# Optimization experiments

Hardware: AMD Instinct MI355X
Metric: run time of the kernel (lower is better)

## Reference

```python
import jax, jax.numpy as jnp
import numpy as np

HIDDEN = 1024
HEADS = 16
HEAD_DIM = HIDDEN // HEADS
SCALE = float(np.sqrt(HEAD_DIM))


def setup_inputs() -> dict:
    key = jax.random.key(0)
    ks = jax.random.split(key, 9)
    B, S = 4, 8192
    std = 1.0 / np.sqrt(HIDDEN)
    x = jax.random.normal(ks[0], (B, S, HIDDEN), dtype=jnp.float32)
    Wq = jax.random.normal(ks[1], (HIDDEN, HIDDEN), dtype=jnp.float32) * std
    Wk = jax.random.normal(ks[2], (HIDDEN, HIDDEN), dtype=jnp.float32) * std
    Wv = jax.random.normal(ks[3], (HIDDEN, HIDDEN), dtype=jnp.float32) * std
    Wo = jax.random.normal(ks[4], (HIDDEN, HIDDEN), dtype=jnp.float32) * std
    bq = jax.random.normal(ks[5], (HIDDEN,), dtype=jnp.float32) * std
    bk = jax.random.normal(ks[6], (HIDDEN,), dtype=jnp.float32) * std
    bv = jax.random.normal(ks[7], (HIDDEN,), dtype=jnp.float32) * std
    bo = jax.random.normal(ks[8], (HIDDEN,), dtype=jnp.float32) * std
    return {"x": x, "Wq": Wq, "bq": bq, "Wk": Wk, "bk": bk,
            "Wv": Wv, "bv": bv, "Wo": Wo, "bo": bo}


def reference(x, Wq, bq, Wk, bk, Wv, bv, Wo, bo):
    B, S, E = x.shape
    H, D = HEADS, HEAD_DIM
    # torch nn.Linear: y = x @ W^T + b
    q = (jnp.einsum('bse,fe->bsf', x, Wq) + bq).reshape(B, S, H, D)
    k = (jnp.einsum('bse,fe->bsf', x, Wk) + bk).reshape(B, S, H, D)
    v = (jnp.einsum('bse,fe->bsf', x, Wv) + bv).reshape(B, S, H, D)
    # Faithful to source: NO head transpose, so matmul contracts over head_dim
    # with (B,S) as batch dims -> per-token head-mixing scores [B,S,H,H].
    scores = jnp.einsum('bshd,bsgd->bshg', q, k) / SCALE
    probs = jax.nn.softmax(scores, axis=-1)
    attn = jnp.einsum('bshg,bsgd->bshd', probs, v).reshape(B, S, E)
    return jnp.einsum('bse,fe->bsf', attn, Wo) + bo
```

## Files before the change

### kernel.cpp

```cpp
#include <hip/hip_runtime.h>
#include <hip/hip_bf16.h>
#include <cstdint>
#include <type_traits>

#define GLOBAL_AS __attribute__((address_space(1)))
#define LDS_AS    __attribute__((address_space(3)))

typedef short bf16x8 __attribute__((ext_vector_type(8)));
typedef short short8_t __attribute__((ext_vector_type(8)));
typedef float f32x4  __attribute__((ext_vector_type(4)));

static constexpr int E_DIM = 1024;
static constexpr int HD = 64;
static constexpr int QKV_STRIDE = 3072;
static constexpr int KDIM = 1024;
static constexpr int NTK  = KDIM / 64;
static constexpr int NIT  = NTK / 2;

__device__ __forceinline__ float b2f(short s) {
    union { unsigned u; float f; } x;
    x.u = ((unsigned)(unsigned short)s) << 16;
    return x.f;
}
__device__ __forceinline__ short f2b(float f) {
    union { float f; unsigned u; } x; x.f = f;
    unsigned r = x.u + 0x7FFF + ((x.u >> 16) & 1);
    return (short)(r >> 16);
}

__global__ __launch_bounds__(256) void k_prep(
    const float* __restrict__ x,
    const float* __restrict__ Wq, const float* __restrict__ Wk,
    const float* __restrict__ Wv, const float* __restrict__ Wo,
    const float* __restrict__ bq, const float* __restrict__ bk,
    const float* __restrict__ bv,
    short* __restrict__ xb, short* __restrict__ Wqkvb, short* __restrict__ Wob,
    float* __restrict__ bqkv, int n4x, int n4w)
{
    int i = blockIdx.x * 256 + threadIdx.x;
    const float* src;
    short* dst;
    int j;
    if (i < n4x)                       { src = x;  dst = xb;                  j = i; }
    else if (i < n4x + n4w)            { src = Wq; dst = Wqkvb;               j = i - n4x; }
    else if (i < n4x + 2 * n4w)        { src = Wk; dst = Wqkvb + 4 * n4w;     j = i - n4x - n4w; }
    else if (i < n4x + 3 * n4w)        { src = Wv; dst = Wqkvb + 8 * n4w;     j = i - n4x - 2 * n4w; }
    else if (i < n4x + 4 * n4w)        { src = Wo; dst = Wob;                 j = i - n4x - 3 * n4w; }
    else {
        int b = i - (n4x + 4 * n4w);
        if (b < 768) {
            #pragma unroll
            for (int e = 0; e < 4; ++e) {
                int idx = b * 4 + e;
                float v = (idx < 1024) ? bq[idx] : (idx < 2048 ? bk[idx - 1024] : bv[idx - 2048]);
                bqkv[idx] = v;
            }
        }
        return;
    }
    float4 v = reinterpret_cast<const float4*>(src)[j];
    short4 o;
    o.x = f2b(v.x); o.y = f2b(v.y); o.z = f2b(v.z); o.w = f2b(v.w);
    reinterpret_cast<short4*>(dst)[j] = o;
}

template <typename OutT>
__global__ __launch_bounds__(512, 2) void k_gemm256(
    const short* __restrict__ A,
    const short* __restrict__ Bm,
    const float* __restrict__ bias,
    OutT* __restrict__ C,
    int NT_N, int N)
{
    __shared__ short lds[65536];

    const int tid  = threadIdx.x;
    const int lane = tid & 63;
    const int wv   = tid >> 6;
    const int wr   = wv >> 2;
    const int wc   = wv & 3;
    const int frow = lane & 15;
    const int ks   = lane >> 4;
    const int sw   = frow & 7;
    const int sl0  = ((0 + ks) ^ sw) * 8;
    const int sl1  = ((4 + ks) ^ sw) * 8;

    const int nwg = gridDim.x, nper = nwg >> 3, bid = blockIdx.x;
    const int swz = (bid & 7) * nper + (bid >> 3);
    const int m0  = (swz / NT_N) * 256;
    const int n0  = (swz % NT_N) * 256;

    const int ArdBase = wr * 8192;
    const int BrdBase = 16384 + (wc >> 1) * 8192 + (wc & 1) * 4096;

    const int srow = tid >> 3;
    const int ssl  = ((tid & 7) ^ (srow & 7)) * 8;
    const int sdst = tid * 8;

#define GLD(SRC, DST) __builtin_amdgcn_global_load_lds(                            \
        (const GLOBAL_AS short*)(SRC), (LDS_AS short*)(DST), 16, 0, 0)
#define STAGE_A(BUF, HALF, T) do {                                                 \
    const short* s_ = A + (size_t)(m0 + (HALF) * 128 + srow) * KDIM + (T) * 64 + ssl; \
    short* d_ = &lds[(BUF) * 32768 + (HALF) * 8192 + sdst];                        \
    GLD(s_, d_);  GLD(s_ + (size_t)64 * KDIM, d_ + 4096);                          \
} while (0)
#define STAGE_B(BUF, HALF, T) do {                                                 \
    const short* s_ = Bm + (size_t)(n0 + (HALF) * 128 + srow) * KDIM + (T) * 64 + ssl; \
    short* d_ = &lds[(BUF) * 32768 + 16384 + (HALF) * 8192 + sdst];                \
    GLD(s_, d_);  GLD(s_ + (size_t)64 * KDIM, d_ + 4096);                          \
} while (0)

#define RD_A(BUF, MIB) do {                                                        \
    _Pragma("unroll")                                                              \
    for (int m_ = 0; m_ < 4; ++m_) {                                               \
        const short* p_ = &lds[(BUF) * 32768 + ArdBase + ((MIB) + m_) * 1024 + frow * 64]; \
        af[m_][0] = *(const bf16x8*)(p_ + sl0);                                    \
        af[m_][1] = *(const bf16x8*)(p_ + sl1);                                    \
    }                                                                              \
} while (0)
#define RD_B(BUF, NIB, BF) do {                                                    \
    _Pragma("unroll")                                                              \
    for (int n_ = 0; n_ < 2; ++n_) {                                               \
        const short* p_ = &lds[(BUF) * 32768 + BrdBase + ((NIB) + n_) * 1024 + frow * 64]; \
        BF[n_][0] = *(const bf16x8*)(p_ + sl0);                                    \
        BF[n_][1] = *(const bf16x8*)(p_ + sl1);                                    \
    }                                                                              \
} while (0)

#define MM(MB, NB, BF) do {                                                        \
    _Pragma("unroll")                                                              \
    for (int m_ = 0; m_ < 4; ++m_)                                                 \
        _Pragma("unroll")                                                          \
        for (int n_ = 0; n_ < 2; ++n_) {                                           \
            acc[(MB)+m_][(NB)+n_] = __builtin_amdgcn_mfma_f32_16x16x32_bf16(       \
                af[m_][0], BF[n_][0], acc[(MB)+m_][(NB)+n_], 0, 0, 0);             \
            acc[(MB)+m_][(NB)+n_] = __builtin_amdgcn_mfma_f32_16x16x32_bf16(       \
                af[m_][1], BF[n_][1], acc[(MB)+m_][(NB)+n_], 0, 0, 0);             \
        }                                                                          \
} while (0)

#define BAR   __builtin_amdgcn_s_barrier()
#define LGKM0 asm volatile("s_waitcnt lgkmcnt(0)")
#define LGKM8 asm volatile("s_waitcnt lgkmcnt(8)")
#define VM4   asm volatile("s_waitcnt vmcnt(4)" ::: "memory")
#define PRIO1 __builtin_amdgcn_s_setprio(1)
#define PRIO0 __builtin_amdgcn_s_setprio(0)

    f32x4 acc[8][4];
    #pragma unroll
    for (int i = 0; i < 8; ++i)
        #pragma unroll
        for (int j = 0; j < 4; ++j)
            acc[i][j] = (f32x4){0.f, 0.f, 0.f, 0.f};

    bf16x8 af[4][2], bfA[2][2], bfB[2][2];

    STAGE_B(0, 0, 0);  STAGE_B(0, 1, 0);
    STAGE_A(0, 0, 0);  STAGE_A(0, 1, 0);
    STAGE_B(1, 0, 1);  STAGE_B(1, 1, 1);
    VM4;  BAR;

    #pragma unroll 1
    for (int it = 0; it < NIT; ++it) {
        const int ta = 2 * it + 1;
        const int tb = (2 * it + 2 <= 15) ? 2 * it + 2 : 15;
        const int tc = (2 * it + 3 <= 15) ? 2 * it + 3 : 15;

        RD_A(0, 0);  RD_B(0, 0, bfA);
        STAGE_A(1, 0, ta);
        LGKM8;  BAR;  LGKM0;
        PRIO1;  MM(0, 0, bfA);  PRIO0;  BAR;
        RD_B(0, 2, bfB);
        STAGE_A(1, 1, ta);
        BAR;  LGKM0;
        PRIO1;  MM(0, 2, bfB);  PRIO0;  BAR;
        RD_A(0, 4);
        STAGE_B(0, 0, tb);
        BAR;  LGKM0;
        PRIO1;  MM(4, 0, bfA);  PRIO0;  BAR;
        STAGE_B(0, 1, tb);
        BAR;
        PRIO1;  MM(4, 2, bfB);  PRIO0;
        VM4;  BAR;

        RD_A(1, 0);  RD_B(1, 0, bfA);
        STAGE_A(0, 0, tb);
        LGKM8;  BAR;  LGKM0;
        PRIO1;  MM(0, 0, bfA);  PRIO0;  BAR;
        RD_B(1, 2, bfB);
        STAGE_A(0, 1, tb);
        BAR;  LGKM0;
        PRIO1;  MM(0, 2, bfB);  PRIO0;  BAR;
        RD_A(1, 4);
        STAGE_B(1, 0, tc);
        BAR;  LGKM0;
        PRIO1;  MM(4, 0, bfA);  PRIO0;  BAR;
        STAGE_B(1, 1, tc);
        BAR;
        PRIO1;  MM(4, 2, bfB);  PRIO0;
        VM4;  BAR;
    }

    asm volatile("s_waitcnt vmcnt(0)" ::: "memory");

    const int crow = (lane >> 4) * 4;
    const int ccol = lane & 15;
    float bv4[4];
    #pragma unroll
    for (int ni = 0; ni < 4; ++ni)
        bv4[ni] = bias[n0 + wc * 64 + ni * 16 + ccol];
    #pragma unroll
    for (int mi = 0; mi < 8; ++mi) {
        #pragma unroll
        for (int r = 0; r < 4; ++r) {
            const size_t rowg = (size_t)(m0 + wr * 128 + mi * 16 + crow + r) * N;
            #pragma unroll
            for (int ni = 0; ni < 4; ++ni) {
                const int col = n0 + wc * 64 + ni * 16 + ccol;
                float v = acc[mi][ni][r] + bv4[ni];
                if constexpr (std::is_same<OutT, float>::value) {
                    C[rowg + col] = v;
                } else {
                    C[rowg + col] = f2b(v);
                }
            }
        }
    }
#undef GLD
#undef STAGE_A
#undef STAGE_B
#undef RD_A
#undef RD_B
#undef MM
#undef BAR
#undef LGKM0
#undef LGKM8
#undef VM4
#undef PRIO1
#undef PRIO0
}

__global__ __launch_bounds__(256) void k_attn(
    const short* __restrict__ QKV, short* __restrict__ O)
{
    __shared__ short Ks[16][1032];
    __shared__ short Vs[16][1032];

    const int tid = threadIdx.x;
    const int tok0 = blockIdx.x * 16;

    for (int i = tid; i < 2048; i += 256) {
        int t = i >> 7;
        int j = i & 127;
        const size_t base = (size_t)(tok0 + t) * QKV_STRIDE;
        *reinterpret_cast<short8_t*>(&Ks[t][j * 8]) =
            *reinterpret_cast<const short8_t*>(&QKV[base + 1024 + j * 8]);
        *reinterpret_cast<short8_t*>(&Vs[t][j * 8]) =
            *reinterpret_cast<const short8_t*>(&QKV[base + 2048 + j * 8]);
    }
    __syncthreads();

    const int tl = tid >> 4;
    const int h  = tid & 15;

    float qf[64];
    const short* qp = QKV + (size_t)(tok0 + tl) * QKV_STRIDE + h * HD;
    #pragma unroll
    for (int i = 0; i < 8; ++i) {
        short8_t v = *reinterpret_cast<const short8_t*>(&qp[i * 8]);
        #pragma unroll
        for (int j = 0; j < 8; ++j) qf[i * 8 + j] = b2f(v[j]);
    }

    float s[16];
    #pragma unroll
    for (int g = 0; g < 16; ++g) {
        float a = 0.f;
        #pragma unroll
        for (int i = 0; i < 8; ++i) {
            short8_t kv = *reinterpret_cast<const short8_t*>(&Ks[tl][g * HD + i * 8]);
            #pragma unroll
            for (int j = 0; j < 8; ++j) a += qf[i * 8 + j] * b2f(kv[j]);
        }
        s[g] = a * 0.125f;
    }
    float mx = s[0];
    #pragma unroll
    for (int g = 1; g < 16; ++g) mx = fmaxf(mx, s[g]);
    float l = 0.f;
    #pragma unroll
    for (int g = 0; g < 16; ++g) { s[g] = __expf(s[g] - mx); l += s[g]; }
    const float inv = 1.f / l;
    #pragma unroll
    for (int g = 0; g < 16; ++g) s[g] *= inv;

    short* op = O + (size_t)(tok0 + tl) * E_DIM + h * HD;
    #pragma unroll
    for (int c = 0; c < 4; ++c) {
        float a[16];
        #pragma unroll
        for (int j = 0; j < 16; ++j) a[j] = 0.f;
        #pragma unroll
        for (int g = 0; g < 16; ++g) {
            short8_t v0 = *reinterpret_cast<const short8_t*>(&Vs[tl][g * HD + c * 16]);
            short8_t v1 = *reinterpret_cast<const short8_t*>(&Vs[tl][g * HD + c * 16 + 8]);
            #pragma unroll
            for (int j = 0; j < 8; ++j) {
                a[j]     += s[g] * b2f(v0[j]);
                a[8 + j] += s[g] * b2f(v1[j]);
            }
        }
        short8_t o0, o1;
        #pragma unroll
        for (int j = 0; j < 8; ++j) { o0[j] = f2b(a[j]); o1[j] = f2b(a[8 + j]); }
        *reinterpret_cast<short8_t*>(&op[c * 16])     = o0;
        *reinterpret_cast<short8_t*>(&op[c * 16 + 8]) = o1;
    }
}

extern "C" void kernel_launch(void* const* d_in, const int* in_sizes, int n_in,
                              void* d_out, int out_size, void* d_ws, size_t ws_size,
                              hipStream_t stream) {
    const float* x  = (const float*)d_in[0];
    const float* Wq = (const float*)d_in[1];
    const float* bq = (const float*)d_in[2];
    const float* Wk = (const float*)d_in[3];
    const float* bk = (const float*)d_in[4];
    const float* Wv = (const float*)d_in[5];
    const float* bv = (const float*)d_in[6];
    const float* Wo = (const float*)d_in[7];
    const float* bo = (const float*)d_in[8];
    float* out = (float*)d_out;

    const int T = in_sizes[0] / E_DIM;
    char* ws = (char*)d_ws;
    const size_t SZ_X    = (size_t)T * E_DIM * 2;
    const size_t SZ_WQKV = (size_t)3 * E_DIM * E_DIM * 2;
    const size_t SZ_W    = (size_t)E_DIM * E_DIM * 2;
    const size_t SZ_B    = 3072 * sizeof(float) + 4096;

    short* xb    = (short*)(ws);
    short* Wqkvb = (short*)(ws + SZ_X);
    short* Wob   = (short*)(ws + SZ_X + SZ_WQKV);
    float* bqkv  = (float*)(ws + SZ_X + SZ_WQKV + SZ_W);
    short* QKVb  = (short*)(ws + SZ_X + SZ_WQKV + SZ_W + SZ_B);
    short* Ab    = xb;

    const int n4x = T * E_DIM / 4;
    const int n4w = E_DIM * E_DIM / 4;
    const int nprep = n4x + 4 * n4w + 768;
    k_prep<<<dim3((nprep + 255) / 256), dim3(256), 0, stream>>>(
        x, Wq, Wk, Wv, Wo, bq, bk, bv, xb, Wqkvb, Wob, bqkv, n4x, n4w);

    k_gemm256<short><<<dim3((T / 256) * (QKV_STRIDE / 256)), dim3(512), 0, stream>>>(
        xb, Wqkvb, bqkv, QKVb, QKV_STRIDE / 256, QKV_STRIDE);

    k_attn<<<dim3(T / 16), dim3(256), 0, stream>>>(QKVb, Ab);

    k_gemm256<float><<<dim3((T / 256) * (E_DIM / 256)), dim3(512), 0, stream>>>(
        Ab, Wob, bo, out, E_DIM / 256, E_DIM);
}
```

Measured before the change: 393.0 us.

## Software-pipeline LDS fragment reads across iterations and drop explicit lgkmcnt waits

Restructures the GEMM main loop so the first A/B fragment reads and the next A stage of each half-iteration are issued at the end of the previous phase, with a prologue that preloads them. It removes the explicit lgkmcnt waits and about half of the barriers, relying on the compiler to insert LDS waits. The setprio calls move into the MFMA macro. This aims to cut synchronization stalls and overlap LDS reads with MFMA work, but it risks ordering hazards: reusing buffers with fewer barriers could race, and the stage issued on the last iteration reads a clamped tile it never uses.

Measured after the change: 387.7 us (median of 2 runs). Within noise of the previous version (-1.3%).

```diff
diff --git a/kernel.cpp b/kernel.cpp
--- a/kernel.cpp
+++ b/kernel.cpp
@@ -128,6 +128,7 @@
 } while (0)
 
 #define MM(MB, NB, BF) do {                                                        \
+    __builtin_amdgcn_s_setprio(1);                                                 \
     _Pragma("unroll")                                                              \
     for (int m_ = 0; m_ < 4; ++m_)                                                 \
         _Pragma("unroll")                                                          \
@@ -137,14 +138,12 @@
             acc[(MB)+m_][(NB)+n_] = __builtin_amdgcn_mfma_f32_16x16x32_bf16(       \
                 af[m_][1], BF[n_][1], acc[(MB)+m_][(NB)+n_], 0, 0, 0);             \
         }                                                                          \
+    __builtin_amdgcn_s_setprio(0);                                                 \
 } while (0)
 
 #define BAR   __builtin_amdgcn_s_barrier()
-#define LGKM0 asm volatile("s_waitcnt lgkmcnt(0)")
-#define LGKM8 asm volatile("s_waitcnt lgkmcnt(8)")
 #define VM4   asm volatile("s_waitcnt vmcnt(4)" ::: "memory")
-#define PRIO1 __builtin_amdgcn_s_setprio(1)
-#define PRIO0 __builtin_amdgcn_s_setprio(0)
+#define VM6   asm volatile("s_waitcnt vmcnt(6)" ::: "memory")
 
     f32x4 acc[8][4];
     #pragma unroll
@@ -158,7 +157,9 @@
     STAGE_B(0, 0, 0);  STAGE_B(0, 1, 0);
     STAGE_A(0, 0, 0);  STAGE_A(0, 1, 0);
     STAGE_B(1, 0, 1);  STAGE_B(1, 1, 1);
-    VM4;  BAR;
+    STAGE_A(1, 0, 1);
+    VM6;  BAR;
+    RD_A(0, 0);  RD_B(0, 0, bfA);
 
     #pragma unroll 1
     for (int it = 0; it < NIT; ++it) {
@@ -166,39 +167,38 @@
         const int tb = (2 * it + 2 <= 15) ? 2 * it + 2 : 15;
         const int tc = (2 * it + 3 <= 15) ? 2 * it + 3 : 15;
 
-        RD_A(0, 0);  RD_B(0, 0, bfA);
-        STAGE_A(1, 0, ta);
-        LGKM8;  BAR;  LGKM0;
-        PRIO1;  MM(0, 0, bfA);  PRIO0;  BAR;
+        BAR;
+        MM(0, 0, bfA);
         RD_B(0, 2, bfB);
         STAGE_A(1, 1, ta);
-        BAR;  LGKM0;
-        PRIO1;  MM(0, 2, bfB);  PRIO0;  BAR;
+        BAR;
+        MM(0, 2, bfB);
         RD_A(0, 4);
         STAGE_B(0, 0, tb);
-        BAR;  LGKM0;
-        PRIO1;  MM(4, 0, bfA);  PRIO0;  BAR;
+        BAR;
+        MM(4, 0, bfA);
         STAGE_B(0, 1, tb);
-        BAR;
-        PRIO1;  MM(4, 2, bfB);  PRIO0;
-        VM4;  BAR;
-
+        VM4;
+        BAR;
+        MM(4, 2, bfB);
         RD_A(1, 0);  RD_B(1, 0, bfA);
         STAGE_A(0, 0, tb);
-        LGKM8;  BAR;  LGKM0;
-        PRIO1;  MM(0, 0, bfA);  PRIO0;  BAR;
+        BAR;
+        MM(0, 0, bfA);
         RD_B(1, 2, bfB);
         STAGE_A(0, 1, tb);
-        BAR;  LGKM0;
-        PRIO1;  MM(0, 2, bfB);  PRIO0;  BAR;
+        BAR;
+        MM(0, 2, bfB);
         RD_A(1, 4);
         STAGE_B(1, 0, tc);
-        BAR;  LGKM0;
-        PRIO1;  MM(4, 0, bfA);  PRIO0;  BAR;
+        BAR;
+        MM(4, 0, bfA);
         STAGE_B(1, 1, tc);
-        BAR;
-        PRIO1;  MM(4, 2, bfB);  PRIO0;
-        VM4;  BAR;
+        VM4;
+        BAR;
+        MM(4, 2, bfB);
+        RD_A(0, 0);  RD_B(0, 0, bfA);
+        STAGE_A(1, 0, tc);
     }
 
     asm volatile("s_waitcnt vmcnt(0)" ::: "memory");
@@ -233,11 +233,8 @@
 #undef RD_B
 #undef MM
 #undef BAR
-#undef LGKM0
-#undef LGKM8
 #undef VM4
-#undef PRIO1
-#undef PRIO0
+#undef VM6
 }
 
 __global__ __launch_bounds__(256) void k_attn(
```
